# Kernel tuning notes

Measured on AMD Instinct MI355X. Metric: run time of the kernel, lower is better.

Reference implementation:

```python
import jax, jax.numpy as jnp
import numpy as np

N = 8192
D_IN = 3
D_K = 128
HID = 256
N_RES = 2
N_TRI = 2730
N_EDGE = 2048
EPS = float(jnp.finfo(jnp.float32).eps)  # torch RMSNorm default eps=None -> finfo eps


def setup_inputs() -> dict:
    key = jax.random.key(0)
    ks = jax.random.split(key, 16)
    std = 0.02
    inp = {
        "edge_features": jax.random.normal(ks[0], (N, D_IN), dtype=jnp.float32),
        "edge_ids": jax.random.randint(ks[1], (N,), 0, N_EDGE),
        "triangle_ids": jax.random.randint(ks[2], (N,), 0, N_TRI),
        # projections (stored as [in, out]; equivalent to torch Linear)
        "Wq": jax.random.normal(ks[3], (D_IN, D_K), dtype=jnp.float32) * std,
        "bq": jnp.zeros((D_K,), jnp.float32),
        "Wk": jax.random.normal(ks[4], (D_IN, D_K), dtype=jnp.float32) * std,
        "bk": jnp.zeros((D_K,), jnp.float32),
        "Wv": jax.random.normal(ks[5], (D_IN, D_K), dtype=jnp.float32) * std,
        "bv": jnp.zeros((D_K,), jnp.float32),
        # attention MLP: Linear(d_k, hid) -> N_RES ResBlocks -> Linear(hid, 1)
        "W0": jax.random.normal(ks[6], (D_K, HID), dtype=jnp.float32) * std,
        "b0": jnp.zeros((HID,), jnp.float32),
        "rms_w": jnp.ones((N_RES, HID), jnp.float32),
        "Wres": jax.random.normal(ks[7], (N_RES, HID, HID), dtype=jnp.float32) * std,
        "bres": jnp.zeros((N_RES, HID), jnp.float32),
        "Wout": jax.random.normal(ks[8], (HID, 1), dtype=jnp.float32) * std,
        "bout": jnp.zeros((1,), jnp.float32),
    }
    return inp


def _rmsnorm(x, g):
    ms = jnp.mean(x * x, axis=-1, keepdims=True)
    return x * jax.lax.rsqrt(ms + EPS) * g


def reference(edge_features, edge_ids, triangle_ids,
              Wq, bq, Wk, bk, Wv, bv,
              W0, b0, rms_w, Wres, bres, Wout, bout):
    q = edge_features @ Wq + bq          # [N, d_k]
    k = edge_features @ Wk + bk
    v = edge_features @ Wv + bv
    scores = (q @ k.T) / jnp.sqrt(jnp.float32(D_K))   # [N, N]
    mask = triangle_ids[:, None] == triangle_ids[None, :]
    scores = jnp.where(mask, scores, -jnp.inf)
    attn = jax.nn.softmax(scores, axis=1)             # every row has diag True
    attended = attn @ v                                # [N, d_k]
    # MLP with ResBlocks
    h = attended @ W0 + b0                             # [N, hid]
    for i in range(N_RES):
        h = h + jax.nn.relu(_rmsnorm(h, rms_w[i]) @ Wres[i] + bres[i])
    logits = (h @ Wout + bout)[:, 0]                   # [N]
    # scatter_softmax over edge_ids (dim=0)
    seg_max = jax.ops.segment_max(logits, edge_ids, num_segments=N_EDGE)
    ex = jnp.exp(logits - seg_max[edge_ids])
    seg_sum = jax.ops.segment_sum(ex, edge_ids, num_segments=N_EDGE)
    weights = ex / seg_sum[edge_ids]
    return weights
```

## Files before the change

kernel.cpp:

```cpp
#include <hip/hip_runtime.h>
#include <math.h>

#define N 8192
#define D_IN 3
#define D_K 128
#define HID 256
#define N_RES 2
#define N_TRI 2730
#define N_EDGE 2048
#define EPS 1.1920929e-07f

typedef unsigned short u16;
typedef unsigned int u32;
typedef float f32x4 __attribute__((ext_vector_type(4)));
typedef short s16x8 __attribute__((ext_vector_type(8)));

#define OFF_LOGITS   0
#define OFF_TRIOFF   32768
#define OFF_TRICNT   43776
#define OFF_MEF      54784
#define OFF_SEGS     185856
#define OFF_WPK      194048
#define OFF_WV0      456192
#define OFF_B0P      459264
#define OFF_ATTC     460288

__device__ __forceinline__ u16 f2bf(float f) {
    u32 u = __float_as_uint(f);
    u32 r = (u + 0x7fffu + ((u >> 16) & 1u)) >> 16;
    return (u16)r;
}

__global__ __launch_bounds__(1024) void k_setup(
        const float* __restrict__ ef, const int* __restrict__ tri,
        const float* __restrict__ Wq, const float* __restrict__ bq,
        const float* __restrict__ Wk, const float* __restrict__ bk,
        const float* __restrict__ Wv, const float* __restrict__ bv,
        const float* __restrict__ W0, const float* __restrict__ b0,
        const float* __restrict__ Wres,
        int* __restrict__ tri_off, int* __restrict__ tri_cnt,
        float* __restrict__ mem_ef,
        u16* __restrict__ Wpk, float* __restrict__ Wv0, float* __restrict__ b0p,
        float* __restrict__ attc, float* __restrict__ seg_sum) {
    if (blockIdx.x == 17) {
        int t = threadIdx.x;
        for (int i = t; i < N_EDGE; i += 1024) seg_sum[i] = 0.f;
        if (t < 256) {
            float a0 = 0.f, a1 = 0.f, a2 = 0.f, ab = 0.f;
            for (int d = 0; d < D_K; ++d) {
                float wc = W0[d * HID + t];
                a0 += Wv[d] * wc;
                a1 += Wv[D_K + d] * wc;
                a2 += Wv[2 * D_K + d] * wc;
                ab += bv[d] * wc;
            }
            Wv0[t] = a0; Wv0[256 + t] = a1; Wv0[512 + t] = a2;
            b0p[t] = ab + b0[t];
        } else if (t < 272) {
            int idx = t - 256;
            float acc = 0.f;
            if (idx < 9) {
                int a = idx / 3, b = idx % 3;
                for (int d = 0; d < D_K; ++d) acc += Wq[a * D_K + d] * Wk[b * D_K + d];
            } else if (idx < 12) {
                int a = idx - 9;
                for (int d = 0; d < D_K; ++d) acc += Wq[a * D_K + d] * bk[d];
            } else if (idx < 15) {
                int b = idx - 12;
                for (int d = 0; d < D_K; ++d) acc += bq[d] * Wk[b * D_K + d];
            } else {
                for (int d = 0; d < D_K; ++d) acc += bq[d] * bk[d];
            }
            attc[idx] = acc;
        }
        return;
    }
    if (blockIdx.x != 0) {
        int tg = (blockIdx.x - 1) * 1024 + threadIdx.x;
        int tile = tg >> 6, lane = tg & 63;
        int q = lane >> 4, c = lane & 15;
        int r = tile >> 7, tl = tile & 127;
        int nt = tl >> 3, kt = tl & 7;
        int k0 = kt * 32 + q * 8, n = nt * 16 + c;
        const float* W = Wres + r * 65536;
        u16 tmp[8];
        #pragma unroll
        for (int j = 0; j < 8; ++j) tmp[j] = f2bf(W[(k0 + j) * HID + n]);
        int dst = r * 65536 + (tl * 64 + lane) * 8;
        *(s16x8*)&Wpk[dst] = *(s16x8*)tmp;
        return;
    }
    __shared__ int sc[4096];
    __shared__ int wp[16];
    const int t = threadIdx.x, lane = t & 63, wid = t >> 6;
    for (int i = t; i < 4096; i += 1024) sc[i] = 0;
    __syncthreads();
    for (int n = t; n < N; n += 1024) atomicAdd(&sc[tri[n]], 1);
    __syncthreads();
    int a0 = sc[t*4], a1 = sc[t*4+1], a2 = sc[t*4+2], a3 = sc[t*4+3];
    int c0 = a0, c1 = c0 + a1, c2 = c1 + a2, c3 = c2 + a3;
    int ts = c3;
    #pragma unroll
    for (int o = 1; o < 64; o <<= 1) { int u = __shfl_up(ts, o); if (lane >= o) ts += u; }
    if (lane == 63) wp[wid] = ts;
    __syncthreads();
    if (wid == 0) {
        int v = (lane < 16) ? wp[lane] : 0;
        #pragma unroll
        for (int o = 1; o < 16; o <<= 1) { int u = __shfl_up(v, o); if (lane >= o) v += u; }
        if (lane < 16) wp[lane] = v;
    }
    __syncthreads();
    {
        int wexcl = wid ? wp[wid - 1] : 0;
        int texcl = wexcl + ts - c3;
        int o0 = texcl, o1 = texcl + c0, o2 = texcl + c1, o3 = texcl + c2;
        if (t*4+0 < N_TRI) { tri_off[t*4+0] = o0; tri_cnt[t*4+0] = a0; }
        if (t*4+1 < N_TRI) { tri_off[t*4+1] = o1; tri_cnt[t*4+1] = a1; }
        if (t*4+2 < N_TRI) { tri_off[t*4+2] = o2; tri_cnt[t*4+2] = a2; }
        if (t*4+3 < N_TRI) { tri_off[t*4+3] = o3; tri_cnt[t*4+3] = a3; }
        sc[t*4+0] = o0; sc[t*4+1] = o1; sc[t*4+2] = o2; sc[t*4+3] = o3;
    }
    __syncthreads();
    for (int n = t; n < N; n += 1024) {
        int p = atomicAdd(&sc[tri[n]], 1);
        f32x4 v = { ef[n*3+0], ef[n*3+1], ef[n*3+2], 0.f };
        *(f32x4*)&mem_ef[p * 4] = v;
    }
}

__global__ __launch_bounds__(512) void k_fused(
        const float* __restrict__ ef, const int* __restrict__ tri,
        const int* __restrict__ eids,
        const int* __restrict__ tri_off, const int* __restrict__ tri_cnt,
        const float* __restrict__ mem_ef,
        const float* __restrict__ attc, const float* __restrict__ Wv0,
        const float* __restrict__ b0p, const float* __restrict__ rms_w,
        const float* __restrict__ bres, const float* __restrict__ Wout,
        const float* __restrict__ bout, const u16* __restrict__ Wpk,
        float* __restrict__ expo, float* __restrict__ seg_sum) {
    __shared__ u16 X[16][264];
    __shared__ float red[8][16];
    __shared__ float ebar[16][4];
    const int tid = threadIdx.x;
    const int w = tid >> 6, lane = tid & 63;
    const int q = lane >> 4, c = lane & 15;
    const int base = blockIdx.x * 16;
    const int colb = w * 32 + c;

    {
        const float scale = 0.08838834764831845f;
        const int half = lane >> 5;
        const int i = lane & 31;
        const int lrow = 2 * w + half;
        const int row = base + lrow;
        float e0 = ef[row*3+0], e1 = ef[row*3+1], e2 = ef[row*3+2];
        float t0 = (e0*attc[0] + e1*attc[3] + e2*attc[6] + attc[12]) * scale;
        float t1 = (e0*attc[1] + e1*attc[4] + e2*attc[7] + attc[13]) * scale;
        float t2 = (e0*attc[2] + e1*attc[5] + e2*attc[8] + attc[14]) * scale;
        float tb = (e0*attc[9] + e1*attc[10] + e2*attc[11] + attc[15]) * scale;
        int tt = tri[row];
        int off = tri_off[tt], cnt = tri_cnt[tt];
        float m = -INFINITY, l = 0.f, sa0 = 0.f, sa1 = 0.f, sa2 = 0.f;
        for (int bs = 0; bs < cnt; bs += 32) {
            int nn = cnt - bs; if (nn > 32) nn = 32;
            float f0 = 0.f, f1 = 0.f, f2 = 0.f, s = -INFINITY;
            if (i < nn) {
                f32x4 F = *(const f32x4*)&mem_ef[(off + bs + i) * 4];
                f0 = F[0]; f1 = F[1]; f2 = F[2];
                s = tb + t0*f0 + t1*f1 + t2*f2;
            }
            float m1 = s;
            #pragma unroll
            for (int o = 16; o > 0; o >>= 1) m1 = fmaxf(m1, __shfl_xor(m1, o));
            float p = (i < nn) ? __expf(s - m1) : 0.f;
            float pl = p, p0 = p * f0, p1 = p * f1, p2 = p * f2;
            #pragma unroll
            for (int o = 16; o > 0; o >>= 1) {
                pl += __shfl_xor(pl, o);
                p0 += __shfl_xor(p0, o);
                p1 += __shfl_xor(p1, o);
                p2 += __shfl_xor(p2, o);
            }
            float mn = fmaxf(m, m1);
            float ra = __expf(m - mn);
            float rb = __expf(m1 - mn);
            l   = l   * ra + pl * rb;
            sa0 = sa0 * ra + p0 * rb;
            sa1 = sa1 * ra + p1 * rb;
            sa2 = sa2 * ra + p2 * rb;
            m = mn;
        }
        if (i == 0) {
            float inv = 1.f / l;
            ebar[lrow][0] = sa0 * inv;
            ebar[lrow][1] = sa1 * inv;
            ebar[lrow][2] = sa2 * inv;
        }
    }
    __syncthreads();

    const s16x8* Bp = (const s16x8*)Wpk;
    float h[2][4];
    f32x4 acc[2];
    const f32x4 zero = {0.f, 0.f, 0.f, 0.f};

    #pragma unroll
    for (int nt = 0; nt < 2; ++nt) {
        int col = colb + nt * 16;
        float w0 = Wv0[col], w1 = Wv0[256 + col], w2 = Wv0[512 + col], bb = b0p[col];
        #pragma unroll
        for (int rg = 0; rg < 4; ++rg) {
            int rr = q * 4 + rg;
            h[nt][rg] = bb + ebar[rr][0]*w0 + ebar[rr][1]*w1 + ebar[rr][2]*w2;
        }
    }

    for (int ir = 0; ir < N_RES; ++ir) {
        float part[4];
        #pragma unroll
        for (int rg = 0; rg < 4; ++rg) {
            part[rg] = h[0][rg] * h[0][rg] + h[1][rg] * h[1][rg];
            #pragma unroll
            for (int o = 1; o < 16; o <<= 1) part[rg] += __shfl_xor(part[rg], o);
        }
        if (c == 0) {
            #pragma unroll
            for (int rg = 0; rg < 4; ++rg) red[w][q * 4 + rg] = part[rg];
        }
        __syncthreads();
        float sc4[4];
        #pragma unroll
        for (int rg = 0; rg < 4; ++rg) {
            int rr = q * 4 + rg;
            float ms = (red[0][rr] + red[1][rr] + red[2][rr] + red[3][rr]
                      + red[4][rr] + red[5][rr] + red[6][rr] + red[7][rr]) * (1.f / HID);
            sc4[rg] = rsqrtf(ms + EPS);
        }
        #pragma unroll
        for (int nt = 0; nt < 2; ++nt) {
            float gg = rms_w[ir * HID + colb + nt * 16];
            #pragma unroll
            for (int rg = 0; rg < 4; ++rg)
                X[q * 4 + rg][colb + nt * 16] = f2bf(h[nt][rg] * sc4[rg] * gg);
        }
        __syncthreads();

        const s16x8* Br = Bp + ir * 8192;
        #pragma unroll
        for (int nt = 0; nt < 2; ++nt) acc[nt] = zero;
        #pragma unroll
        for (int kt = 0; kt < 8; ++kt) {
            s16x8 a = *(const s16x8*)&X[c][kt * 32 + q * 8];
            #pragma unroll
            for (int nt = 0; nt < 2; ++nt) {
                s16x8 b = Br[((w * 2 + nt) * 8 + kt) * 64 + lane];
                acc[nt] = __builtin_amdgcn_mfma_f32_16x16x32_bf16(a, b, acc[nt], 0, 0, 0);
            }
        }
        #pragma unroll
        for (int nt = 0; nt < 2; ++nt) {
            float bb = bres[ir * HID + colb + nt * 16];
            #pragma unroll
            for (int rg = 0; rg < 4; ++rg) h[nt][rg] += fmaxf(acc[nt][rg] + bb, 0.f);
        }
    }

    {
        float wo0 = Wout[colb], wo1 = Wout[colb + 16];
        float part[4];
        #pragma unroll
        for (int rg = 0; rg < 4; ++rg) {
            part[rg] = h[0][rg] * wo0 + h[1][rg] * wo1;
            #pragma unroll
            for (int o = 1; o < 16; o <<= 1) part[rg] += __shfl_xor(part[rg], o);
        }
        if (c == 0) {
            #pragma unroll
            for (int rg = 0; rg < 4; ++rg) red[w][q * 4 + rg] = part[rg];
        }
        __syncthreads();
        if (tid < 16) {
            float s = bout[0];
            #pragma unroll
            for (int w2 = 0; w2 < 8; ++w2) s += red[w2][tid];
            float p = __expf(s);
            expo[base + tid] = p;
            atomicAdd(&seg_sum[eids[base + tid]], p);
        }
    }
}

__global__ __launch_bounds__(256) void k_out(
        const float* __restrict__ expo, const int* __restrict__ eids,
        const float* __restrict__ seg_sum, float* __restrict__ out) {
    int n = blockIdx.x * 256 + threadIdx.x;
    out[n] = expo[n] / seg_sum[eids[n]];
}

extern "C" void kernel_launch(void* const* d_in, const int* in_sizes, int n_in,
                              void* d_out, int out_size, void* d_ws, size_t ws_size,
                              hipStream_t stream) {
    const float* ef   = (const float*)d_in[0];
    const int*   eids = (const int*)d_in[1];
    const int*   tri  = (const int*)d_in[2];
    const float* Wq = (const float*)d_in[3];
    const float* bq = (const float*)d_in[4];
    const float* Wk = (const float*)d_in[5];
    const float* bk = (const float*)d_in[6];
    const float* Wv = (const float*)d_in[7];
    const float* bv = (const float*)d_in[8];
    const float* W0 = (const float*)d_in[9];
    const float* b0 = (const float*)d_in[10];
    const float* rms_w = (const float*)d_in[11];
    const float* Wres  = (const float*)d_in[12];
    const float* bres  = (const float*)d_in[13];
    const float* Wout  = (const float*)d_in[14];
    const float* bout  = (const float*)d_in[15];
    float* out = (float*)d_out;

    char* ws = (char*)d_ws;
    float* expo    = (float*)(ws + OFF_LOGITS);
    int*   tri_off = (int*)(ws + OFF_TRIOFF);
    int*   tri_cnt = (int*)(ws + OFF_TRICNT);
    float* mem_ef  = (float*)(ws + OFF_MEF);
    float* seg_sum = (float*)(ws + OFF_SEGS);
    u16*   Wpk     = (u16*)(ws + OFF_WPK);
    float* Wv0     = (float*)(ws + OFF_WV0);
    float* b0p     = (float*)(ws + OFF_B0P);
    float* attc    = (float*)(ws + OFF_ATTC);

    hipLaunchKernelGGL(k_setup, dim3(18), dim3(1024), 0, stream,
                       ef, tri, Wq, bq, Wk, bk, Wv, bv, W0, b0, Wres,
                       tri_off, tri_cnt, mem_ef, Wpk, Wv0, b0p, attc, seg_sum);
    hipLaunchKernelGGL(k_fused, dim3(N / 16), dim3(512), 0, stream,
                       ef, tri, eids, tri_off, tri_cnt, mem_ef,
                       attc, Wv0, b0p, rms_w, bres, Wout, bout, Wpk,
                       expo, seg_sum);
    hipLaunchKernelGGL(k_out, dim3(N / 256), dim3(256), 0, stream,
                       expo, eids, seg_sum, out);
}
```

Baseline: 111.2 us.

## Process 32 rows per block with 16 waves, each wave owning 16 columns

The fused MLP block now handles 32 rows with 1024 threads instead of 16 rows with 512 threads. Each wave owns one 16-column tile across two 16-row tiles, so every B-fragment load from the packed weights feeds two MFMAs. This halves per-row weight traffic from global/L2. In exchange the grid is halved to 256 blocks and the reductions span 16 waves, which may reduce occupancy and lengthen the attention prologue per block.

Result: slower. 116.0 us (+4.3%).

```diff
diff --git a/kernel.cpp b/kernel.cpp
--- a/kernel.cpp
+++ b/kernel.cpp
@@ -129,7 +129,7 @@
     }
 }
 
-__global__ __launch_bounds__(512) void k_fused(
+__global__ __launch_bounds__(1024) void k_fused(
         const float* __restrict__ ef, const int* __restrict__ tri,
         const int* __restrict__ eids,
         const int* __restrict__ tri_off, const int* __restrict__ tri_cnt,
@@ -139,14 +139,14 @@
         const float* __restrict__ bres, const float* __restrict__ Wout,
         const float* __restrict__ bout, const u16* __restrict__ Wpk,
         float* __restrict__ expo, float* __restrict__ seg_sum) {
-    __shared__ u16 X[16][264];
-    __shared__ float red[8][16];
-    __shared__ float ebar[16][4];
+    __shared__ u16 X[32][264];
+    __shared__ float red[16][32];
+    __shared__ float ebar[32][4];
     const int tid = threadIdx.x;
     const int w = tid >> 6, lane = tid & 63;
     const int q = lane >> 4, c = lane & 15;
-    const int base = blockIdx.x * 16;
-    const int colb = w * 32 + c;
+    const int base = blockIdx.x * 32;
+    const int colb = w * 16 + c;
 
     {
         const float scale = 0.08838834764831845f;
@@ -205,85 +205,101 @@
     f32x4 acc[2];
     const f32x4 zero = {0.f, 0.f, 0.f, 0.f};
 
-    #pragma unroll
-    for (int nt = 0; nt < 2; ++nt) {
-        int col = colb + nt * 16;
-        float w0 = Wv0[col], w1 = Wv0[256 + col], w2 = Wv0[512 + col], bb = b0p[col];
-        #pragma unroll
-        for (int rg = 0; rg < 4; ++rg) {
-            int rr = q * 4 + rg;
-            h[nt][rg] = bb + ebar[rr][0]*w0 + ebar[rr][1]*w1 + ebar[rr][2]*w2;
+    {
+        float w0 = Wv0[colb], w1 = Wv0[256 + colb], w2 = Wv0[512 + colb], bb = b0p[colb];
+        #pragma unroll
+        for (int rt = 0; rt < 2; ++rt) {
+            #pragma unroll
+            for (int rg = 0; rg < 4; ++rg) {
+                int rr = rt * 16 + q * 4 + rg;
+                h[rt][rg] = bb + ebar[rr][0]*w0 + ebar[rr][1]*w1 + ebar[rr][2]*w2;
+            }
         }
     }
 
     for (int ir = 0; ir < N_RES; ++ir) {
-        float part[4];
-        #pragma unroll
-        for (int rg = 0; rg < 4; ++rg) {
-            part[rg] = h[0][rg] * h[0][rg] + h[1][rg] * h[1][rg];
-            #pragma unroll
-            for (int o = 1; o < 16; o <<= 1) part[rg] += __shfl_xor(part[rg], o);
+        float part[2][4];
+        #pragma unroll
+        for (int rt = 0; rt < 2; ++rt) {
+            #pragma unroll
+            for (int rg = 0; rg < 4; ++rg) {
+                part[rt][rg] = h[rt][rg] * h[rt][rg];
+                #pragma unroll
+                for (int o = 1; o < 16; o <<= 1) part[rt][rg] += __shfl_xor(part[rt][rg], o);
+            }
         }
         if (c == 0) {
             #pragma unroll
-            for (int rg = 0; rg < 4; ++rg) red[w][q * 4 + rg] = part[rg];
+            for (int rt = 0; rt < 2; ++rt)
+                #pragma unroll
+                for (int rg = 0; rg < 4; ++rg) red[w][rt * 16 + q * 4 + rg] = part[rt][rg];
         }
         __syncthreads();
-        float sc4[4];
-        #pragma unroll
-        for (int rg = 0; rg < 4; ++rg) {
-            int rr = q * 4 + rg;
-            float ms = (red[0][rr] + red[1][rr] + red[2][rr] + red[3][rr]
-                      + red[4][rr] + red[5][rr] + red[6][rr] + red[7][rr]) * (1.f / HID);
-            sc4[rg] = rsqrtf(ms + EPS);
-        }
-        #pragma unroll
-        for (int nt = 0; nt < 2; ++nt) {
-            float gg = rms_w[ir * HID + colb + nt * 16];
-            #pragma unroll
-            for (int rg = 0; rg < 4; ++rg)
-                X[q * 4 + rg][colb + nt * 16] = f2bf(h[nt][rg] * sc4[rg] * gg);
+        float sc4[2][4];
+        #pragma unroll
+        for (int rt = 0; rt < 2; ++rt) {
+            #pragma unroll
+            for (int rg = 0; rg < 4; ++rg) {
+                int rr = rt * 16 + q * 4 + rg;
+                float ms = 0.f;
+                #pragma unroll
+                for (int w2 = 0; w2 < 16; ++w2) ms += red[w2][rr];
+                sc4[rt][rg] = rsqrtf(ms * (1.f / HID) + EPS);
+            }
+        }
+        {
+            float gg = rms_w[ir * HID + colb];
+            #pragma unroll
+            for (int rt = 0; rt < 2; ++rt)
+                #pragma unroll
+                for (int rg = 0; rg < 4; ++rg)
+                    X[rt * 16 + q * 4 + rg][colb] = f2bf(h[rt][rg] * sc4[rt][rg] * gg);
         }
         __syncthreads();
 
         const s16x8* Br = Bp + ir * 8192;
         #pragma unroll
-        for (int nt = 0; nt < 2; ++nt) acc[nt] = zero;
+        for (int rt = 0; rt < 2; ++rt) acc[rt] = zero;
         #pragma unroll
         for (int kt = 0; kt < 8; ++kt) {
-            s16x8 a = *(const s16x8*)&X[c][kt * 32 + q * 8];
-            #pragma unroll
-            for (int nt = 0; nt < 2; ++nt) {
-                s16x8 b = Br[((w * 2 + nt) * 8 + kt) * 64 + lane];
-                acc[nt] = __builtin_amdgcn_mfma_f32_16x16x32_bf16(a, b, acc[nt], 0, 0, 0);
-            }
-        }
-        #pragma unroll
-        for (int nt = 0; nt < 2; ++nt) {
-            float bb = bres[ir * HID + colb + nt * 16];
-            #pragma unroll
-            for (int rg = 0; rg < 4; ++rg) h[nt][rg] += fmaxf(acc[nt][rg] + bb, 0.f);
+            s16x8 b = Br[(w * 8 + kt) * 64 + lane];
+            s16x8 a0 = *(const s16x8*)&X[c][kt * 32 + q * 8];
+            s16x8 a1 = *(const s16x8*)&X[16 + c][kt * 32 + q * 8];
+            acc[0] = __builtin_amdgcn_mfma_f32_16x16x32_bf16(a0, b, acc[0], 0, 0, 0);
+            acc[1] = __builtin_amdgcn_mfma_f32_16x16x32_bf16(a1, b, acc[1], 0, 0, 0);
+        }
+        {
+            float bb = bres[ir * HID + colb];
+            #pragma unroll
+            for (int rt = 0; rt < 2; ++rt)
+                #pragma unroll
+                for (int rg = 0; rg < 4; ++rg) h[rt][rg] += fmaxf(acc[rt][rg] + bb, 0.f);
         }
     }
 
     {
-        float wo0 = Wout[colb], wo1 = Wout[colb + 16];
-        float part[4];
-        #pragma unroll
-        for (int rg = 0; rg < 4; ++rg) {
-            part[rg] = h[0][rg] * wo0 + h[1][rg] * wo1;
-            #pragma unroll
-            for (int o = 1; o < 16; o <<= 1) part[rg] += __shfl_xor(part[rg], o);
+        float wo = Wout[colb];
+        float part[2][4];
+        #pragma unroll
+        for (int rt = 0; rt < 2; ++rt) {
+            #pragma unroll
+            for (int rg = 0; rg < 4; ++rg) {
+                part[rt][rg] = h[rt][rg] * wo;
+                #pragma unroll
+                for (int o = 1; o < 16; o <<= 1) part[rt][rg] += __shfl_xor(part[rt][rg], o);
+            }
         }
         if (c == 0) {
             #pragma unroll
-            for (int rg = 0; rg < 4; ++rg) red[w][q * 4 + rg] = part[rg];
+            for (int rt = 0; rt < 2; ++rt)
+                #pragma unroll
+                for (int rg = 0; rg < 4; ++rg) red[w][rt * 16 + q * 4 + rg] = part[rt][rg];
         }
         __syncthreads();
-        if (tid < 16) {
+        if (tid < 32) {
             float s = bout[0];
             #pragma unroll
-            for (int w2 = 0; w2 < 8; ++w2) s += red[w2][tid];
+            for (int w2 = 0; w2 < 16; ++w2) s += red[w2][tid];
             float p = __expf(s);
             expo[base + tid] = p;
             atomicAdd(&seg_sum[eids[base + tid]], p);
@@ -333,7 +349,7 @@
     hipLaunchKernelGGL(k_setup, dim3(18), dim3(1024), 0, stream,
                        ef, tri, Wq, bq, Wk, bk, Wv, bv, W0, b0, Wres,
                        tri_off, tri_cnt, mem_ef, Wpk, Wv0, b0p, attc, seg_sum);
-    hipLaunchKernelGGL(k_fused, dim3(N / 16), dim3(512), 0, stream,
+    hipLaunchKernelGGL(k_fused, dim3(N / 32), dim3(1024), 0, stream,
                        ef, tri, eids, tri_off, tri_cnt, mem_ef,
                        attc, Wv0, b0p, rms_w, bres, Wout, bout, Wpk,
                        expo, seg_sum);
```
